# Kernel optimization log

Measured on AMD Instinct MI355X. Metric: run time of the kernel, lower is better.

## Reference

```python
import jax, jax.numpy as jnp
import numpy as np

B, T, C = 32, 1024, 256   # T must equal block_size for the mask broadcast to be valid
HS = 64                   # head_size


def setup_inputs() -> dict:
    key = jax.random.key(0)
    kx, kk, kq, kv = jax.random.split(key, 4)
    s = 1.0 / np.sqrt(C)  # nn.Linear default-ish scale
    return {
        "x": jax.random.normal(kx, (B, T, C), dtype=jnp.float32),
        "Wk": jax.random.uniform(kk, (HS, C), dtype=jnp.float32, minval=-s, maxval=s),
        "Wq": jax.random.uniform(kq, (HS, C), dtype=jnp.float32, minval=-s, maxval=s),
        "Wv": jax.random.uniform(kv, (HS, C), dtype=jnp.float32, minval=-s, maxval=s),
    }


def reference(x, Wk, Wq, Wv):
    # projections: nn.Linear(bias=False) -> x @ W^T
    k = jnp.einsum('btc,hc->bth', x, Wk)  # [B,T,HS]
    q = jnp.einsum('btc,hc->bth', x, Wq)
    v = jnp.einsum('btc,hc->bth', x, Wv)
    # fresh cache + T == block_size  =>  k_cache = k, v_cache = v
    wei = jnp.einsum('bth,bsh->bts', q, k) / np.sqrt(HS)  # [B,T,T]
    causal = jnp.tril(jnp.ones((T, T), dtype=bool))
    wei = jnp.where(causal, wei, -jnp.inf)
    wei = jax.nn.softmax(wei, axis=-1)  # dropout p=0 -> identity
    out = jnp.einsum('bts,bsh->bth', wei, v)  # [B,T,HS]
    return out
```

## Files before the change

### kernel.cpp

```cpp
#include <hip/hip_runtime.h>
#include <hip/hip_bf16.h>
#include <math.h>


#define B_  32
#define T_  1024
#define C_  256
#define HS_ 64
#define QSCALE 0.1803368801111204f

typedef __attribute__((ext_vector_type(8))) short bf16x8;
typedef __attribute__((ext_vector_type(4))) float f32x4;

static __device__ __forceinline__ unsigned short f2bf(float f) {
    unsigned u = __builtin_bit_cast(unsigned, f);
    u += 0x7FFFu + ((u >> 16) & 1u);
    return (unsigned short)(u >> 16);
}
static __device__ __forceinline__ unsigned pack_bf2(float a, float b) {
    unsigned ua = __builtin_bit_cast(unsigned, a) + 0x8000u;
    unsigned ub = __builtin_bit_cast(unsigned, b) + 0x8000u;
    return __builtin_amdgcn_perm(ub, ua, 0x07060302u);
}
static __device__ __forceinline__ float fexp2(float x) {
#if __has_builtin(__builtin_amdgcn_exp2f)
    return __builtin_amdgcn_exp2f(x);
#else
    return exp2f(x);
#endif
}

__global__ __launch_bounds__(256) void prep_kernel(
    const float* __restrict__ Wk, const float* __restrict__ Wq,
    const float* __restrict__ Wv, unsigned short* __restrict__ wbf)
{
    const int idx = blockIdx.x * 256 + threadIdx.x;
    const int row = idx >> 6, c4 = (idx & 63) << 2;
    const float* src; float sc = 1.0f;
    if (row < 64)       src = &Wk[(size_t)row * C_];
    else if (row < 128) { src = &Wq[(size_t)(row - 64) * C_]; sc = QSCALE; }
    else                src = &Wv[(size_t)(row - 128) * C_];
    float4 v = *(const float4*)&src[c4];
    uint2 o = make_uint2(pack_bf2(v.x * sc, v.y * sc), pack_bf2(v.z * sc, v.w * sc));
    *(uint2*)&wbf[(size_t)row * C_ + c4] = o;
}

__global__ __launch_bounds__(256) void proj_kernel(
    const float* __restrict__ x, const unsigned short* __restrict__ wbf,
    unsigned short* __restrict__ fqk, unsigned short* __restrict__ vt)
{
    const int tid = threadIdx.x;
    const int lane = tid & 63, w = tid >> 6;
    const int wm = w & 1, wn = w >> 1;
    const int q4 = lane >> 4, l15 = lane & 15;
    const int mbase = blockIdx.x * 64 + wm * 32;

    f32x4 acc[6][2];
    #pragma unroll
    for (int nt = 0; nt < 6; ++nt)
        #pragma unroll
        for (int mt = 0; mt < 2; ++mt) acc[nt][mt] = (f32x4)0.0f;

    for (int c0 = 0; c0 < C_; c0 += 32) {
        bf16x8 bx[2];
        #pragma unroll
        for (int mt = 0; mt < 2; ++mt) {
            const float* px = &x[(size_t)(mbase + mt * 16 + l15) * C_ + c0 + q4 * 8];
            float4 v0 = *(const float4*)px;
            float4 v1 = *(const float4*)(px + 4);
            union { bf16x8 v; unsigned u[4]; } t;
            t.u[0] = pack_bf2(v0.x, v0.y); t.u[1] = pack_bf2(v0.z, v0.w);
            t.u[2] = pack_bf2(v1.x, v1.y); t.u[3] = pack_bf2(v1.z, v1.w);
            bx[mt] = t.v;
        }
        #pragma unroll
        for (int nt = 0; nt < 6; ++nt) {
            bf16x8 a = *(const bf16x8*)&wbf[(size_t)(wn * 96 + nt * 16 + l15) * C_ + c0 + q4 * 8];
            #pragma unroll
            for (int mt = 0; mt < 2; ++mt)
                acc[nt][mt] = __builtin_amdgcn_mfma_f32_16x16x32_bf16(a, bx[mt], acc[nt][mt], 0, 0, 0);
        }
    }

    #pragma unroll
    for (int nt = 0; nt < 6; ++nt) {
        const int nbase = wn * 96 + nt * 16 + q4 * 4;
        #pragma unroll
        for (int mt = 0; mt < 2; ++mt) {
            const int m = mbase + mt * 16 + l15;
            f32x4 v = acc[nt][mt];
            if (nbase < 128) {
                uint2 o = make_uint2(pack_bf2(v.x, v.y), pack_bf2(v.z, v.w));
                *(uint2*)&fqk[(size_t)m * 128 + nbase] = o;
            } else {
                const int batch = m >> 10, s = m & 1023, h = nbase - 128;
                vt[((size_t)batch * 64 + h + 0) * 1024 + s] = f2bf(v.x);
                vt[((size_t)batch * 64 + h + 1) * 1024 + s] = f2bf(v.y);
                vt[((size_t)batch * 64 + h + 2) * 1024 + s] = f2bf(v.z);
                vt[((size_t)batch * 64 + h + 3) * 1024 + s] = f2bf(v.w);
            }
        }
    }
}

__global__ __launch_bounds__(256) void attn_kernel(
    const unsigned short* __restrict__ fqk,
    const unsigned short* __restrict__ vt,
    float* __restrict__ out)
{
    __shared__ __align__(16) char smem[34816];

    const int tid = threadIdx.x;
    const int lane = tid & 63, w = tid >> 6;
    const int q4 = lane >> 4, l15 = lane & 15;
    const int batch = blockIdx.x & 31;
    const int qt = 31 - (blockIdx.x >> 5);
    const int q0 = qt * 32;
    const int ns = (qt >> 1) + 1;

    unsigned short (*Ps)[72] = (unsigned short(*)[72])(smem + w * 4608);

    bf16x8 qf[2][2];
    #pragma unroll
    for (int it = 0; it < 2; ++it)
        #pragma unroll
        for (int kc = 0; kc < 2; ++kc)
            qf[it][kc] = *(const bf16x8*)&fqk[(size_t)(batch * T_ + q0 + it * 16 + l15) * 128 + 64 + kc * 32 + q4 * 8];

    f32x4 o[4][2];
    #pragma unroll
    for (int ht = 0; ht < 4; ++ht)
        #pragma unroll
        for (int it = 0; it < 2; ++it) o[ht][it] = (f32x4)0.0f;
    float l[2] = {0.f, 0.f};

    const unsigned short* kbase = &fqk[(size_t)(batch * T_) * 128];
    const unsigned short* vbase = &vt[(size_t)batch * 64 * 1024];

    for (int st = w; st < ns; st += 4) {
        const int s0 = st * 64;
        const bool last = (st == ns - 1);
        #pragma unroll
        for (int hf = 0; hf < 2; ++hf) {
            const int sh = s0 + hf * 32;
            bf16x8 ak[2][2];
            #pragma unroll
            for (int st16 = 0; st16 < 2; ++st16)
                #pragma unroll
                for (int kc = 0; kc < 2; ++kc)
                    ak[st16][kc] = *(const bf16x8*)&kbase[(size_t)(sh + st16 * 16 + l15) * 128 + kc * 32 + q4 * 8];
            bf16x8 av[4];
            #pragma unroll
            for (int ht = 0; ht < 4; ++ht)
                av[ht] = *(const bf16x8*)&vbase[(size_t)(ht * 16 + l15) * 1024 + sh + q4 * 8];
            f32x4 s[2][2];
            #pragma unroll
            for (int st16 = 0; st16 < 2; ++st16)
                #pragma unroll
                for (int it = 0; it < 2; ++it) {
                    f32x4 c = (f32x4)0.0f;
                    c = __builtin_amdgcn_mfma_f32_16x16x32_bf16(ak[st16][0], qf[it][0], c, 0, 0, 0);
                    c = __builtin_amdgcn_mfma_f32_16x16x32_bf16(ak[st16][1], qf[it][1], c, 0, 0, 0);
                    s[st16][it] = c;
                }
            #pragma unroll
            for (int st16 = 0; st16 < 2; ++st16)
                #pragma unroll
                for (int it = 0; it < 2; ++it) {
                    const int iloc = it * 16 + l15;
                    float p[4];
                    #pragma unroll
                    for (int r = 0; r < 4; ++r) {
                        float pv = fexp2(s[st16][it][r]);
                        if (last) {
                            int sl = sh + st16 * 16 + q4 * 4 + r;
                            if (sl > q0 + iloc) pv = 0.0f;
                        }
                        p[r] = pv;
                        l[it] += pv;
                    }
                    uint2 pw = make_uint2(pack_bf2(p[0], p[1]), pack_bf2(p[2], p[3]));
                    *(uint2*)&Ps[iloc][hf * 32 + st16 * 16 + q4 * 4] = pw;
                }
            #pragma unroll
            for (int it = 0; it < 2; ++it) {
                bf16x8 bp = *(const bf16x8*)&Ps[it * 16 + l15][hf * 32 + q4 * 8];
                #pragma unroll
                for (int ht = 0; ht < 4; ++ht)
                    o[ht][it] = __builtin_amdgcn_mfma_f32_16x16x32_bf16(av[ht], bp, o[ht][it], 0, 0, 0);
            }
        }
    }

    #pragma unroll
    for (int it = 0; it < 2; ++it) {
        l[it] += __shfl_xor(l[it], 16);
        l[it] += __shfl_xor(l[it], 32);
    }

    __syncthreads();
    float4* ocomb = (float4*)smem;
    float*  lcomb = (float*)(smem + 32768);
    #pragma unroll
    for (int ht = 0; ht < 4; ++ht)
        #pragma unroll
        for (int it = 0; it < 2; ++it) {
            f32x4 v = o[ht][it];
            ocomb[((w * 4 + ht) * 2 + it) * 64 + lane] = make_float4(v.x, v.y, v.z, v.w);
        }
    #pragma unroll
    for (int it = 0; it < 2; ++it) lcomb[(w * 2 + it) * 64 + lane] = l[it];
    __syncthreads();

    #pragma unroll
    for (int it = 0; it < 2; ++it) {
        float4 a = make_float4(0.f, 0.f, 0.f, 0.f);
        float lt = 0.f;
        #pragma unroll
        for (int src = 0; src < 4; ++src) {
            float4 t = ocomb[((src * 4 + w) * 2 + it) * 64 + lane];
            a.x += t.x; a.y += t.y; a.z += t.z; a.w += t.w;
            lt += lcomb[(src * 2 + it) * 64 + lane];
        }
        float inv = 1.0f / lt;
        float4 res = make_float4(a.x * inv, a.y * inv, a.z * inv, a.w * inv);
        *(float4*)&out[(size_t)(batch * T_ + q0 + it * 16 + l15) * HS_ + w * 16 + q4 * 4] = res;
    }
}

extern "C" void kernel_launch(void* const* d_in, const int* in_sizes, int n_in,
                              void* d_out, int out_size, void* d_ws, size_t ws_size,
                              hipStream_t stream) {
    (void)in_sizes; (void)n_in; (void)out_size; (void)ws_size;
    const float* x  = (const float*)d_in[0];
    const float* Wk = (const float*)d_in[1];
    const float* Wq = (const float*)d_in[2];
    const float* Wv = (const float*)d_in[3];

    unsigned short* wbf = (unsigned short*)d_ws;
    unsigned short* fqk = (unsigned short*)((char*)d_ws + 98304);
    unsigned short* vtb = (unsigned short*)((char*)d_ws + 98304 + (size_t)32768 * 128 * 2);

    hipLaunchKernelGGL(prep_kernel, dim3(48),   dim3(256), 0, stream, Wk, Wq, Wv, wbf);
    hipLaunchKernelGGL(proj_kernel, dim3(512),  dim3(256), 0, stream, x, wbf, fqk, vtb);
    hipLaunchKernelGGL(attn_kernel, dim3(1024), dim3(256), 0, stream, fqk, vtb, (float*)d_out);
}
```

Baseline: 121.6 us.

## Fuse weight bf16 conversion into projection kernel and retile to 32-row blocks

Removes the separate weight-preparation kernel and converts fp32 weights to bf16 (with the Q scale folded in) directly inside the projection loop. The projection block tile shrinks from 64 to 32 rows, each wave now owns 48 output columns, and the grid doubles to 1024 blocks, with an occupancy hint added. This saves one kernel launch and a workspace round trip, but every block now reads fp32 weights, doubling weight traffic and adding per-iteration conversion work.

```diff
diff --git a/kernel.cpp b/kernel.cpp
--- a/kernel.cpp
+++ b/kernel.cpp
@@ -21,6 +21,16 @@
     unsigned ua = __builtin_bit_cast(unsigned, a) + 0x8000u;
     unsigned ub = __builtin_bit_cast(unsigned, b) + 0x8000u;
     return __builtin_amdgcn_perm(ub, ua, 0x07060302u);
+}
+static __device__ __forceinline__ bf16x8 cvt8(const float* p, float sc) {
+    float4 v0 = *(const float4*)p;
+    float4 v1 = *(const float4*)(p + 4);
+    union { bf16x8 v; unsigned u[4]; } t;
+    t.u[0] = pack_bf2(v0.x * sc, v0.y * sc);
+    t.u[1] = pack_bf2(v0.z * sc, v0.w * sc);
+    t.u[2] = pack_bf2(v1.x * sc, v1.y * sc);
+    t.u[3] = pack_bf2(v1.z * sc, v1.w * sc);
+    return t.v;
 }
 static __device__ __forceinline__ float fexp2(float x) {
 #if __has_builtin(__builtin_amdgcn_exp2f)
@@ -30,64 +40,53 @@
 #endif
 }
 
-__global__ __launch_bounds__(256) void prep_kernel(
+__global__ __launch_bounds__(256, 4) void proj_kernel(
+    const float* __restrict__ x,
     const float* __restrict__ Wk, const float* __restrict__ Wq,
-    const float* __restrict__ Wv, unsigned short* __restrict__ wbf)
-{
-    const int idx = blockIdx.x * 256 + threadIdx.x;
-    const int row = idx >> 6, c4 = (idx & 63) << 2;
-    const float* src; float sc = 1.0f;
-    if (row < 64)       src = &Wk[(size_t)row * C_];
-    else if (row < 128) { src = &Wq[(size_t)(row - 64) * C_]; sc = QSCALE; }
-    else                src = &Wv[(size_t)(row - 128) * C_];
-    float4 v = *(const float4*)&src[c4];
-    uint2 o = make_uint2(pack_bf2(v.x * sc, v.y * sc), pack_bf2(v.z * sc, v.w * sc));
-    *(uint2*)&wbf[(size_t)row * C_ + c4] = o;
-}
-
-__global__ __launch_bounds__(256) void proj_kernel(
-    const float* __restrict__ x, const unsigned short* __restrict__ wbf,
+    const float* __restrict__ Wv,
     unsigned short* __restrict__ fqk, unsigned short* __restrict__ vt)
 {
     const int tid = threadIdx.x;
     const int lane = tid & 63, w = tid >> 6;
-    const int wm = w & 1, wn = w >> 1;
     const int q4 = lane >> 4, l15 = lane & 15;
-    const int mbase = blockIdx.x * 64 + wm * 32;
-
-    f32x4 acc[6][2];
-    #pragma unroll
-    for (int nt = 0; nt < 6; ++nt)
+    const int m0 = blockIdx.x * 32;
+
+    const float* wrow[3];
+    float wsc[3];
+    #pragma unroll
+    for (int nt = 0; nt < 3; ++nt) {
+        const int nb = 48 * w + nt * 16;
+        if (nb < 64)       { wrow[nt] = &Wk[(size_t)(nb      + l15) * C_]; wsc[nt] = 1.0f; }
+        else if (nb < 128) { wrow[nt] = &Wq[(size_t)(nb - 64 + l15) * C_]; wsc[nt] = QSCALE; }
+        else               { wrow[nt] = &Wv[(size_t)(nb - 128 + l15) * C_]; wsc[nt] = 1.0f; }
+    }
+    const float* xrow0 = &x[(size_t)(m0 + l15) * C_ + q4 * 8];
+    const float* xrow1 = xrow0 + (size_t)16 * C_;
+
+    f32x4 acc[3][2];
+    #pragma unroll
+    for (int nt = 0; nt < 3; ++nt)
         #pragma unroll
         for (int mt = 0; mt < 2; ++mt) acc[nt][mt] = (f32x4)0.0f;
 
+    #pragma unroll 2
     for (int c0 = 0; c0 < C_; c0 += 32) {
-        bf16x8 bx[2];
+        bf16x8 bx0 = cvt8(xrow0 + c0, 1.0f);
+        bf16x8 bx1 = cvt8(xrow1 + c0, 1.0f);
+        #pragma unroll
+        for (int nt = 0; nt < 3; ++nt) {
+            bf16x8 a = cvt8(wrow[nt] + c0 + q4 * 8, wsc[nt]);
+            acc[nt][0] = __builtin_amdgcn_mfma_f32_16x16x32_bf16(a, bx0, acc[nt][0], 0, 0, 0);
+            acc[nt][1] = __builtin_amdgcn_mfma_f32_16x16x32_bf16(a, bx1, acc[nt][1], 0, 0, 0);
+        }
+    }
+
+    #pragma unroll
+    for (int nt = 0; nt < 3; ++nt) {
+        const int nbase = 48 * w + nt * 16 + q4 * 4;
         #pragma unroll
         for (int mt = 0; mt < 2; ++mt) {
-            const float* px = &x[(size_t)(mbase + mt * 16 + l15) * C_ + c0 + q4 * 8];
-            float4 v0 = *(const float4*)px;
-            float4 v1 = *(const float4*)(px + 4);
-            union { bf16x8 v; unsigned u[4]; } t;
-            t.u[0] = pack_bf2(v0.x, v0.y); t.u[1] = pack_bf2(v0.z, v0.w);
-            t.u[2] = pack_bf2(v1.x, v1.y); t.u[3] = pack_bf2(v1.z, v1.w);
-            bx[mt] = t.v;
-        }
-        #pragma unroll
-        for (int nt = 0; nt < 6; ++nt) {
-            bf16x8 a = *(const bf16x8*)&wbf[(size_t)(wn * 96 + nt * 16 + l15) * C_ + c0 + q4 * 8];
-            #pragma unroll
-            for (int mt = 0; mt < 2; ++mt)
-                acc[nt][mt] = __builtin_amdgcn_mfma_f32_16x16x32_bf16(a, bx[mt], acc[nt][mt], 0, 0, 0);
-        }
-    }
-
-    #pragma unroll
-    for (int nt = 0; nt < 6; ++nt) {
-        const int nbase = wn * 96 + nt * 16 + q4 * 4;
-        #pragma unroll
-        for (int mt = 0; mt < 2; ++mt) {
-            const int m = mbase + mt * 16 + l15;
+            const int m = m0 + mt * 16 + l15;
             f32x4 v = acc[nt][mt];
             if (nbase < 128) {
                 uint2 o = make_uint2(pack_bf2(v.x, v.y), pack_bf2(v.z, v.w));
@@ -237,11 +236,11 @@
     const float* Wq = (const float*)d_in[2];
     const float* Wv = (const float*)d_in[3];
 
-    unsigned short* wbf = (unsigned short*)d_ws;
-    unsigned short* fqk = (unsigned short*)((char*)d_ws + 98304);
-    unsigned short* vtb = (unsigned short*)((char*)d_ws + 98304 + (size_t)32768 * 128 * 2);
-
-    hipLaunchKernelGGL(prep_kernel, dim3(48),   dim3(256), 0, stream, Wk, Wq, Wv, wbf);
-    hipLaunchKernelGGL(proj_kernel, dim3(512),  dim3(256), 0, stream, x, wbf, fqk, vtb);
-    hipLaunchKernelGGL(attn_kernel, dim3(1024), dim3(256), 0, stream, fqk, vtb, (float*)d_out);
-}
+    unsigned short* fqk = (unsigned short*)d_ws;
+    unsigned short* vtb = (unsigned short*)((char*)d_ws + (size_t)32768 * 128 * 2);
+
+    hipLaunchKernelGGL(proj_kernel, dim3(1024), dim3(256), 0, stream,
+                       x, Wk, Wq, Wv, fqk, vtb);
+    hipLaunchKernelGGL(attn_kernel, dim3(1024), dim3(256), 0, stream,
+                       fqk, vtb, (float*)d_out);
+}
```

Result: slower. 135.0 us (+11.0%).

## Stage x tile into LDS via direct global-to-LDS loads in projection kernel

Applied to the files above, without the earlier changes.

The projection kernel now loads a 32-row slab of x into LDS with global_load_lds before computing, instead of each wave reading strided float4s from global memory. Work is re-split so each block covers 32 rows and each wave covers 48 output columns, with twice as many blocks. Weight fragments are software-prefetched one k-step ahead. This aims to cut redundant and poorly coalesced global reads of x and raise parallelism, at the cost of 33KB of LDS per block, which limits occupancy.

```diff
diff --git a/kernel.cpp b/kernel.cpp
--- a/kernel.cpp
+++ b/kernel.cpp
@@ -21,6 +21,12 @@
     unsigned ua = __builtin_bit_cast(unsigned, a) + 0x8000u;
     unsigned ub = __builtin_bit_cast(unsigned, b) + 0x8000u;
     return __builtin_amdgcn_perm(ub, ua, 0x07060302u);
+}
+static __device__ __forceinline__ bf16x8 cvt8r(float4 v0, float4 v1) {
+    union { bf16x8 v; unsigned u[4]; } t;
+    t.u[0] = pack_bf2(v0.x, v0.y); t.u[1] = pack_bf2(v0.z, v0.w);
+    t.u[2] = pack_bf2(v1.x, v1.y); t.u[3] = pack_bf2(v1.z, v1.w);
+    return t.v;
 }
 static __device__ __forceinline__ float fexp2(float x) {
 #if __has_builtin(__builtin_amdgcn_exp2f)
@@ -28,6 +34,11 @@
 #else
     return exp2f(x);
 #endif
+}
+static __device__ __forceinline__ void gl_lds16(const float* g, void* l) {
+    __builtin_amdgcn_global_load_lds(
+        (const __attribute__((address_space(1))) unsigned*)g,
+        (__attribute__((address_space(3))) unsigned*)l, 16, 0, 0);
 }
 
 __global__ __launch_bounds__(256) void prep_kernel(
@@ -45,49 +56,72 @@
     *(uint2*)&wbf[(size_t)row * C_ + c4] = o;
 }
 
+#define XPITCH 1040
 __global__ __launch_bounds__(256) void proj_kernel(
     const float* __restrict__ x, const unsigned short* __restrict__ wbf,
     unsigned short* __restrict__ fqk, unsigned short* __restrict__ vt)
 {
+    __shared__ __align__(16) char xls[32 * XPITCH];
+
     const int tid = threadIdx.x;
     const int lane = tid & 63, w = tid >> 6;
-    const int wm = w & 1, wn = w >> 1;
     const int q4 = lane >> 4, l15 = lane & 15;
-    const int mbase = blockIdx.x * 64 + wm * 32;
-
-    f32x4 acc[6][2];
-    #pragma unroll
-    for (int nt = 0; nt < 6; ++nt)
+    const int m0 = blockIdx.x * 32;
+
+    {
+        const float* gbase = &x[(size_t)(m0 + 8 * w) * C_ + lane * 4];
+        #pragma unroll
+        for (int j = 0; j < 8; ++j)
+            gl_lds16(gbase + (size_t)j * C_, xls + (8 * w + j) * XPITCH);
+    }
+
+    const unsigned short* wrow = &wbf[(size_t)(48 * w + l15) * C_ + q4 * 8];
+
+    f32x4 acc[3][2];
+    #pragma unroll
+    for (int nt = 0; nt < 3; ++nt)
         #pragma unroll
         for (int mt = 0; mt < 2; ++mt) acc[nt][mt] = (f32x4)0.0f;
 
-    for (int c0 = 0; c0 < C_; c0 += 32) {
+    bf16x8 aw[3];
+    #pragma unroll
+    for (int nt = 0; nt < 3; ++nt)
+        aw[nt] = *(const bf16x8*)&wrow[(size_t)nt * 16 * C_];
+
+    __syncthreads();
+
+    #pragma unroll
+    for (int ks = 0; ks < 8; ++ks) {
         bf16x8 bx[2];
         #pragma unroll
         for (int mt = 0; mt < 2; ++mt) {
-            const float* px = &x[(size_t)(mbase + mt * 16 + l15) * C_ + c0 + q4 * 8];
-            float4 v0 = *(const float4*)px;
-            float4 v1 = *(const float4*)(px + 4);
-            union { bf16x8 v; unsigned u[4]; } t;
-            t.u[0] = pack_bf2(v0.x, v0.y); t.u[1] = pack_bf2(v0.z, v0.w);
-            t.u[2] = pack_bf2(v1.x, v1.y); t.u[3] = pack_bf2(v1.z, v1.w);
-            bx[mt] = t.v;
-        }
-        #pragma unroll
-        for (int nt = 0; nt < 6; ++nt) {
-            bf16x8 a = *(const bf16x8*)&wbf[(size_t)(wn * 96 + nt * 16 + l15) * C_ + c0 + q4 * 8];
-            #pragma unroll
-            for (int mt = 0; mt < 2; ++mt)
-                acc[nt][mt] = __builtin_amdgcn_mfma_f32_16x16x32_bf16(a, bx[mt], acc[nt][mt], 0, 0, 0);
-        }
-    }
-
-    #pragma unroll
-    for (int nt = 0; nt < 6; ++nt) {
-        const int nbase = wn * 96 + nt * 16 + q4 * 4;
+            const float* p = (const float*)(xls + (mt * 16 + l15) * XPITCH
+                                            + (ks * 32 + q4 * 8) * 4);
+            float4 v0 = *(const float4*)p;
+            float4 v1 = *(const float4*)(p + 4);
+            bx[mt] = cvt8r(v0, v1);
+        }
+        bf16x8 awn[3];
+        if (ks < 7) {
+            #pragma unroll
+            for (int nt = 0; nt < 3; ++nt)
+                awn[nt] = *(const bf16x8*)&wrow[(size_t)nt * 16 * C_ + (ks + 1) * 32];
+        }
+        #pragma unroll
+        for (int nt = 0; nt < 3; ++nt) {
+            acc[nt][0] = __builtin_amdgcn_mfma_f32_16x16x32_bf16(aw[nt], bx[0], acc[nt][0], 0, 0, 0);
+            acc[nt][1] = __builtin_amdgcn_mfma_f32_16x16x32_bf16(aw[nt], bx[1], acc[nt][1], 0, 0, 0);
+        }
+        #pragma unroll
+        for (int nt = 0; nt < 3; ++nt) aw[nt] = awn[nt];
+    }
+
+    #pragma unroll
+    for (int nt = 0; nt < 3; ++nt) {
+        const int nbase = 48 * w + nt * 16 + q4 * 4;
         #pragma unroll
         for (int mt = 0; mt < 2; ++mt) {
-            const int m = mbase + mt * 16 + l15;
+            const int m = m0 + mt * 16 + l15;
             f32x4 v = acc[nt][mt];
             if (nbase < 128) {
                 uint2 o = make_uint2(pack_bf2(v.x, v.y), pack_bf2(v.z, v.w));
@@ -242,6 +276,6 @@
     unsigned short* vtb = (unsigned short*)((char*)d_ws + 98304 + (size_t)32768 * 128 * 2);
 
     hipLaunchKernelGGL(prep_kernel, dim3(48),   dim3(256), 0, stream, Wk, Wq, Wv, wbf);
-    hipLaunchKernelGGL(proj_kernel, dim3(512),  dim3(256), 0, stream, x, wbf, fqk, vtb);
+    hipLaunchKernelGGL(proj_kernel, dim3(1024), dim3(256), 0, stream, x, wbf, fqk, vtb);
     hipLaunchKernelGGL(attn_kernel, dim3(1024), dim3(256), 0, stream, fqk, vtb, (float*)d_out);
 }
```

New measurement: 115.2 us. -5.2%, faster.
